# Performance work log

Measured on AMD Instinct MI355X. Metric: run time of the kernel, lower is better.

## Reference

```python
import jax, jax.numpy as jnp
import numpy as np

MAX_BOXES_PER_IMAGE = 200
NMS_IOU_THRESHOLD = 0.45
CONFIDENCE_THRESHOLD = 0.01
NEG = jnp.float32(-1e9)

B, N, C = 32, 24564, 81  # batch, anchors, classes (incl background)


def setup_inputs() -> dict:
    key = jax.random.key(0)
    k1, k2, k3 = jax.random.split(key, 3)
    logits = jax.random.normal(k1, (B, N, 4 + C), dtype=jnp.float32)
    # anchors in corner format [x0, y0, x1, y1], valid boxes in [0,1]
    centers = jax.random.uniform(k2, (N, 2), dtype=jnp.float32)
    sizes = jax.random.uniform(k3, (N, 2), dtype=jnp.float32) * 0.3 + 0.02
    anchors = jnp.clip(jnp.concatenate([centers - sizes / 2, centers + sizes / 2], axis=-1), 0.0, 1.0)
    return {"logits": logits, "anchors": anchors}


def decode_boxes(loc, anchors):
    # anchors [N,4] corners -> center/size; loc [B,N,4] offsets (no variance scaling, per source)
    cxcy = (anchors[:, 2:4] + anchors[:, 0:2]) / 2  # [N,2]
    wh = anchors[:, 2:4] - anchors[:, 0:2]          # [N,2]
    ctr = loc[..., 0:2] * wh + cxcy                 # [B,N,2]
    sz = jnp.exp(loc[..., 2:4]) * wh                # [B,N,2]
    boxes = jnp.concatenate([ctr - sz / 2, ctr + sz / 2], axis=-1)
    return jnp.clip(boxes, 0.0, 1.0)


def nms_single(boxes, scores):
    # boxes [N,4] corners, scores [N] (already -inf for background / below-threshold)
    area = (boxes[:, 2] - boxes[:, 0]) * (boxes[:, 3] - boxes[:, 1])

    def step(s, _):
        i = jnp.argmax(s)
        keep = s[i] > NEG / 2
        b = boxes[i]
        lt = jnp.maximum(b[:2], boxes[:, :2])
        rb = jnp.minimum(b[2:], boxes[:, 2:])
        whi = jnp.clip(rb - lt, 0.0)
        inter = whi[:, 0] * whi[:, 1]
        iou = inter / (area[i] + area - inter + 1e-9)
        s = jnp.where(iou > NMS_IOU_THRESHOLD, NEG, s).at[i].set(NEG)
        return s, (i, keep)

    _, (idx, keep) = jax.lax.scan(step, scores, None, length=MAX_BOXES_PER_IMAGE)
    return idx, keep  # [M], [M]


def reference(logits, anchors):
    loc = logits[..., :4]
    cls = jax.nn.softmax(logits[..., 4:], axis=-1)          # [B,N,C]
    scores = jnp.max(cls, axis=-1)                           # [B,N]
    classes = jnp.argmax(cls, axis=-1)                       # [B,N]
    boxes = decode_boxes(loc, anchors)                       # [B,N,4]
    # emulate boolean_mask(classes != 0) + score_threshold by masking scores
    valid = (classes != 0) & (scores >= CONFIDENCE_THRESHOLD)
    masked = jnp.where(valid, scores, NEG)
    idx, keep = jax.vmap(nms_single)(boxes, masked)          # [B,M]
    det_boxes = jax.vmap(lambda b, i: b[i])(boxes, idx) * keep[..., None].astype(boxes.dtype)
    det_scores = jax.vmap(lambda s, i: s[i])(scores, idx) * keep.astype(scores.dtype)
    det_classes = jax.vmap(lambda c, i: c[i])(classes, idx) * keep.astype(classes.dtype)
    det_num = jnp.sum(keep, axis=-1).astype(jnp.int32)
    return det_boxes, det_classes, det_scores, det_num
```

## Files before the change

### kernel.cpp

```cpp
#include <hip/hip_runtime.h>

#define Bn 32
#define Nn 24564
#define MAXB 200
#define NBIN 2048
#define CH 2048
#define INVK 0xFFFFFFFFu

typedef unsigned long long u64;
typedef unsigned int u32;

__device__ inline double fast_exp_d(double x) {
  const double LOG2E = 1.4426950408889634074;
  const double LN2   = 0.69314718055994530942;
  double t = x * LOG2E;
  double fi = floor(t + 0.5);
  double f = (t - fi) * LN2;
  double p = 2.505210838544172e-8;
  p = p * f + 2.755731922398589e-7;
  p = p * f + 2.7557319223985893e-6;
  p = p * f + 2.48015873015873e-5;
  p = p * f + 1.984126984126984e-4;
  p = p * f + 1.3888888888888889e-3;
  p = p * f + 8.333333333333333e-3;
  p = p * f + 4.1666666666666664e-2;
  p = p * f + 1.6666666666666666e-1;
  p = p * f + 0.5;
  p = p * f + 1.0;
  p = p * f + 1.0;
  long long e = (long long)fi;
  return p * __longlong_as_double((e + 1023LL) << 52);
}

__device__ inline double clip01(double v) {
  return v < 0.0 ? 0.0 : (v > 1.0 ? 1.0 : v);
}

__global__ __launch_bounds__(256) void r1_score(const float* __restrict__ logits,
                                                u32* __restrict__ keyA) {
  __shared__ float lds[64 * 85];
  const int tid = threadIdx.x;
  const int bx = blockIdx.x;
  const int b = bx / 384;
  const int n0 = (bx % 384) << 6;
  int cnt = Nn - n0;
  cnt = cnt > 64 ? 64 : cnt;
  const int nf4 = (cnt * 85) >> 2;
  const float4* src = reinterpret_cast<const float4*>(logits + ((size_t)b * Nn + n0) * 85);
  float4* dst = reinterpret_cast<float4*>(lds);
  for (int i = tid; i < nf4; i += 256) dst[i] = src[i];
  __syncthreads();

  const int g = tid >> 2;
  const int s = tid & 3;
  if (g < cnt) {
    const float* row = lds + g * 85;
    float mx = -1e30f; int ai = 1000;
    for (int c = s; c < 81; c += 4) {
      float v = row[4 + c];
      if (v > mx) { mx = v; ai = c; }
    }
    #pragma unroll
    for (int d = 1; d <= 2; d <<= 1) {
      float om = __shfl_xor(mx, d);
      int oi = __shfl_xor(ai, d);
      if (om > mx || (om == mx && oi < ai)) { mx = om; ai = oi; }
    }
    float sum = 0.f;
    for (int c = s; c < 81; c += 4) sum += __expf(row[4 + c] - mx);
    sum += __shfl_xor(sum, 1);
    sum += __shfl_xor(sum, 2);
    if (s == 0) {
      float sc = 1.0f / sum;
      u32 kv = INVK;
      if (ai != 0 && sc >= 0.00985f) kv = ~__float_as_uint(sc);
      keyA[(size_t)b * Nn + n0 + g] = kv;
    }
  }
}

__global__ __launch_bounds__(1024) void r2_selnms(const float* __restrict__ logits,
                                                  const float* __restrict__ anchors,
                                                  const u32* __restrict__ keyA,
                                                  double* __restrict__ boxesd,
                                                  int* __restrict__ clsd,
                                                  float* __restrict__ out) {
  __shared__ int hist[NBIN];
  __shared__ int wsum[16];
  __shared__ int clist[CH];
  __shared__ u64 ekeys[CH];
  __shared__ double bb[64][4];
  __shared__ u64 awv[16];
  __shared__ double selBox[MAXB][4];
  __shared__ double selArea[MAXB];
  __shared__ float selScore[MAXB];
  __shared__ int selIdx[MAXB];
  __shared__ int sBinHi, sCnt, sS;

  const int b = blockIdx.x;
  const int tid = threadIdx.x;
  const int lane = tid & 63, wid = tid >> 6;
  const u32* kb = keyA + (size_t)b * Nn;

  for (int i = tid; i < NBIN; i += 1024) hist[i] = 0;
  if (tid == 0) sS = 0;
  __syncthreads();
  for (int i = tid; i < Nn; i += 1024) {
    u32 kv = kb[i];
    u32 bin = (kv - 0xC0000000u) >> 15;
    if (bin < NBIN) atomicAdd(&hist[bin], 1);
  }
  __syncthreads();

  int h0 = hist[2 * tid], h1 = hist[2 * tid + 1];
  int v = h0 + h1;
  int iv = v;
  #pragma unroll
  for (int d = 1; d < 64; d <<= 1) {
    int t = __shfl_up(iv, d);
    if (lane >= d) iv += t;
  }
  if (lane == 63) wsum[wid] = iv;
  __syncthreads();
  if (tid < 16) {
    int w = wsum[tid];
    #pragma unroll
    for (int d = 1; d < 16; d <<= 1) {
      int t = __shfl_up(w, d);
      if ((int)tid >= d) w += t;
    }
    wsum[tid] = w;
  }
  __syncthreads();
  int excl = iv - v + (wid > 0 ? wsum[wid - 1] : 0);
  hist[2 * tid] = excl + h0;
  hist[2 * tid + 1] = excl + h0 + h1;
  __syncthreads();
  const int totalValid = hist[NBIN - 1];

  int binLo = -1, scanBase = 0;
  for (;;) {
    if (sS >= MAXB || scanBase >= totalValid) break;
    if (tid == 0) { sBinHi = binLo; sCnt = 0; }
    __syncthreads();
    {
      const int limit = scanBase + CH;
      int loc = -1;
      if (hist[2 * tid] <= limit) loc = 2 * tid;
      if (hist[2 * tid + 1] <= limit) loc = 2 * tid + 1;
      if (loc > binLo) atomicMax(&sBinHi, loc);
    }
    __syncthreads();
    int binHi = sBinHi;
    if (binHi == binLo) binHi = binLo + 1;

    for (int i0 = 0; i0 < Nn; i0 += 1024) {
      int i = i0 + tid;
      bool pred = false;
      if (i < Nn) {
        u32 kv = kb[i];
        int bin = (int)((kv - 0xC0000000u) >> 15);
        pred = (bin > binLo) && (bin <= binHi);
      }
      u64 m = __ballot(pred);
      int base = 0;
      if (lane == 0 && m) base = atomicAdd(&sCnt, (int)__popcll(m));
      base = __shfl(base, 0);
      if (pred) {
        int off = (int)__popcll(m & ((1ULL << lane) - 1ULL));
        int p = base + off;
        if (p < CH) clist[p] = i;
      }
    }
    __syncthreads();
    int count = sCnt; count = count > CH ? CH : count;
    for (int i = tid; i < CH; i += 1024) ekeys[i] = ~0ULL;
    __syncthreads();

    {
      const int g = tid >> 2, s = tid & 3;
      #pragma unroll 1
      for (int pass = 0; pass < CH / 256; ++pass) {
        int slot = pass * 256 + g;
        if (slot < count) {
          const int n = clist[slot];
          const float* row = logits + ((size_t)b * Nn + n) * 85;
          float rv[21];
          float mx = -1e30f; int ai = 1000;
          #pragma unroll
          for (int q = 0; q < 21; ++q) {
            int cc = s + 4 * q;
            float vv = (cc < 81) ? row[4 + cc] : -1e30f;
            rv[q] = vv;
            if (cc < 81 && vv > mx) { mx = vv; ai = cc; }
          }
          #pragma unroll
          for (int d = 1; d <= 2; d <<= 1) {
            float om = __shfl_xor(mx, d);
            int oi = __shfl_xor(ai, d);
            if (om > mx || (om == mx && oi < ai)) { mx = om; ai = oi; }
          }
          double sum = 0.0;
          #pragma unroll
          for (int q = 0; q < 21; ++q) {
            if (s + 4 * q < 81) sum += fast_exp_d((double)rv[q] - (double)mx);
          }
          sum += __shfl_xor(sum, 1);
          sum += __shfl_xor(sum, 2);
          if (s == 0) {
            u64 K = ~0ULL;
            double score = 1.0 / sum;
            if (ai != 0 && score >= 0.01) {
              float4 a4 = reinterpret_cast<const float4*>(anchors)[n];
              double ax1 = a4.x, ay1 = a4.y, ax2 = a4.z, ay2 = a4.w;
              double cx = (ax2 + ax1) * 0.5, cy = (ay2 + ay1) * 0.5;
              double ww = ax2 - ax1, hh = ay2 - ay1;
              double ctrx = (double)row[0] * ww + cx;
              double ctry = (double)row[1] * hh + cy;
              double szx = fast_exp_d((double)row[2]) * ww;
              double szy = fast_exp_d((double)row[3]) * hh;
              double* bp = boxesd + (size_t)(b * Nn + n) * 4;
              bp[0] = clip01(ctrx - szx * 0.5);
              bp[1] = clip01(ctry - szy * 0.5);
              bp[2] = clip01(ctrx + szx * 0.5);
              bp[3] = clip01(ctry + szy * 0.5);
              clsd[b * Nn + n] = ai;
              u64 sb = (u64)__double_as_longlong(score);
              u64 e4 = (sb >> 52) - 1015ULL;
              u64 mant45 = (sb & ((1ULL << 52) - 1)) >> 7;
              u64 flip = (~((e4 << 45) | mant45)) & ((1ULL << 49) - 1);
              K = (flip << 15) | (u64)n;
            }
            ekeys[slot] = K;
          }
        }
      }
    }
    __syncthreads();

    for (int k = 2; k <= CH; k <<= 1) {
      for (int j = k >> 1; j >= 1; j >>= 1) {
        int l = ((tid & ~(j - 1)) << 1) | (tid & (j - 1));
        int r = l | j;
        bool up = ((l & k) == 0);
        u64 a = ekeys[l], bbv = ekeys[r];
        if ((a > bbv) == up) { ekeys[l] = bbv; ekeys[r] = a; }
        __syncthreads();
      }
    }

    const double THR = 0.45;
    int pos = 0;
    for (;;) {
      int S = sS;
      if (S >= MAXB || pos >= CH) break;
      u64 K = ekeys[pos + lane];
      bool valid = (K != ~0ULL);
      if (!__any(valid)) break;

      if (tid < 256) {
        int c = tid >> 2, comp = tid & 3;
        u64 Kc = ekeys[pos + c];
        double vv = 0.0;
        if (Kc != ~0ULL)
          vv = boxesd[(size_t)(b * Nn + (int)(Kc & 0x7FFF)) * 4 + comp];
        bb[c][comp] = vv;
      }
      __syncthreads();

      double cx1 = bb[lane][0], cy1 = bb[lane][1];
      double cx2 = bb[lane][2], cy2 = bb[lane][3];
      double carea = (cx2 - cx1) * (cy2 - cy1);
      bool aliveL = true;
      for (int k = wid; k < S; k += 16) {
        double ltx = fmax(selBox[k][0], cx1), lty = fmax(selBox[k][1], cy1);
        double rbx = fmin(selBox[k][2], cx2), rby = fmin(selBox[k][3], cy2);
        double w = rbx - ltx; w = w < 0 ? 0 : w;
        double h = rby - lty; h = h < 0 ? 0 : h;
        double inter = w * h;
        double denom = selArea[k] + carea - inter + 1e-9;
        if (inter > THR * denom) aliveL = false;
      }
      u64 aw = __ballot(aliveL);
      if (lane == 0) awv[wid] = aw;
      __syncthreads();

      if (tid < 64) {
        u64 alive = __ballot(valid);
        #pragma unroll
        for (int w = 0; w < 16; ++w) alive &= awv[w];
        u64 m = alive;
        int Sl = S;
        while (m != 0 && Sl < MAXB) {
          int j = __ffsll((unsigned long long)m) - 1;
          double jx1 = bb[j][0], jy1 = bb[j][1], jx2 = bb[j][2], jy2 = bb[j][3];
          double jar = (jx2 - jx1) * (jy2 - jy1);
          u64 Kj = ekeys[pos + j];
          if (lane == 0) {
            u64 key49 = (~(Kj >> 15)) & ((1ULL << 49) - 1);
            u64 e = (key49 >> 45) + 1015ULL;
            u64 mant = (key49 & ((1ULL << 45) - 1)) << 7;
            selBox[Sl][0] = jx1; selBox[Sl][1] = jy1;
            selBox[Sl][2] = jx2; selBox[Sl][3] = jy2;
            selArea[Sl] = jar;
            selScore[Sl] = (float)__longlong_as_double((long long)((e << 52) | mant));
            selIdx[Sl] = (int)(Kj & 0x7FFF);
          }
          Sl++;
          m &= ~(1ULL << j);
          double ltx = fmax(jx1, cx1), lty = fmax(jy1, cy1);
          double rbx = fmin(jx2, cx2), rby = fmin(jy2, cy2);
          double w = rbx - ltx; w = w < 0 ? 0 : w;
          double h = rby - lty; h = h < 0 ? 0 : h;
          double inter = w * h;
          double denom = jar + carea - inter + 1e-9;
          m &= ~__ballot(inter > THR * denom);
        }
        if (lane == 0) sS = Sl;
      }
      __syncthreads();
      pos += 64;
    }
    __syncthreads();
    scanBase = hist[binHi];
    binLo = binHi;
  }

  const int S = sS;
  float* det_boxes = out;
  float* det_classes = out + Bn * MAXB * 4;
  float* det_scores = out + Bn * MAXB * 4 + Bn * MAXB;
  float* det_num = out + Bn * MAXB * 4 + 2 * Bn * MAXB;
  for (int k = tid; k < MAXB; k += 1024) {
    int o = b * MAXB + k;
    if (k < S) {
      det_boxes[o * 4 + 0] = (float)selBox[k][0];
      det_boxes[o * 4 + 1] = (float)selBox[k][1];
      det_boxes[o * 4 + 2] = (float)selBox[k][2];
      det_boxes[o * 4 + 3] = (float)selBox[k][3];
      det_classes[o] = (float)clsd[b * Nn + selIdx[k]];
      det_scores[o] = selScore[k];
    } else {
      det_boxes[o * 4 + 0] = 0.f; det_boxes[o * 4 + 1] = 0.f;
      det_boxes[o * 4 + 2] = 0.f; det_boxes[o * 4 + 3] = 0.f;
      det_classes[o] = 0.f;
      det_scores[o] = 0.f;
    }
  }
  if (tid == 0) det_num[b] = (float)S;
}

extern "C" void kernel_launch(void* const* d_in, const int* in_sizes, int n_in,
                              void* d_out, int out_size, void* d_ws, size_t ws_size,
                              hipStream_t stream) {
  const float* logits = (const float*)d_in[0];
  const float* anchors = (const float*)d_in[1];
  float* out = (float*)d_out;
  char* ws = (char*)d_ws;

  double* boxesd = (double*)ws;
  size_t off = (size_t)Bn * Nn * 4 * sizeof(double);
  int* clsd = (int*)(ws + off);  off += (size_t)Bn * Nn * sizeof(int);
  u32* keyA = (u32*)(ws + off);

  r1_score <<<dim3(Bn * 384), dim3(256),  0, stream>>>(logits, keyA);
  r2_selnms<<<dim3(Bn),       dim3(1024), 0, stream>>>(logits, anchors, keyA,
                                                       boxesd, clsd, out);
}
```

Measured before the change: 187.9 us.

## Split per-image select/NMS kernel into multi-stage grid-parallel pipeline

```diff
diff --git a/kernel.cpp b/kernel.cpp
--- a/kernel.cpp
+++ b/kernel.cpp
@@ -5,6 +5,8 @@
 #define MAXB 200
 #define NBIN 2048
 #define CH 2048
+#define NCHK 4
+#define CHTOT (NCHK * CH)
 #define INVK 0xFFFFFFFFu
 
 typedef unsigned long long u64;
@@ -36,7 +38,7 @@
   return v < 0.0 ? 0.0 : (v > 1.0 ? 1.0 : v);
 }
 
-__global__ __launch_bounds__(256) void r1_score(const float* __restrict__ logits,
+__global__ __launch_bounds__(256) void s1_score(const float* __restrict__ logits,
                                                 u32* __restrict__ keyA) {
   __shared__ float lds[64 * 85];
   const int tid = threadIdx.x;
@@ -79,39 +81,43 @@
   }
 }
 
-__global__ __launch_bounds__(1024) void r2_selnms(const float* __restrict__ logits,
-                                                  const float* __restrict__ anchors,
-                                                  const u32* __restrict__ keyA,
-                                                  double* __restrict__ boxesd,
-                                                  int* __restrict__ clsd,
-                                                  float* __restrict__ out) {
+__global__ __launch_bounds__(256) void s2_hist(const u32* __restrict__ keyA,
+                                               int* __restrict__ histG) {
+  __shared__ int hl[NBIN];
+  const int tid = threadIdx.x;
+  const int bx = blockIdx.x;
+  const int b = bx >> 3;
+  const int sl = (bx & 7) * 3072;
+  for (int i = tid; i < NBIN; i += 256) hl[i] = 0;
+  __syncthreads();
+  const u32* kb = keyA + (size_t)b * Nn;
+  for (int k = 0; k < 12; ++k) {
+    int i = sl + k * 256 + tid;
+    if (i < Nn) {
+      u32 kv = kb[i];
+      u32 bin = (kv - 0xC0000000u) >> 15;
+      if (bin < NBIN) atomicAdd(&hl[bin], 1);
+    }
+  }
+  __syncthreads();
+  for (int i = tid; i < NBIN; i += 256) {
+    int v = hl[i];
+    if (v) atomicAdd(&histG[b * NBIN + i], v);
+  }
+}
+
+__global__ __launch_bounds__(1024) void s3_cut(const int* __restrict__ histG,
+                                               int* __restrict__ chunkIdG,
+                                               int* __restrict__ chunkCntG) {
   __shared__ int hist[NBIN];
   __shared__ int wsum[16];
-  __shared__ int clist[CH];
-  __shared__ u64 ekeys[CH];
-  __shared__ double bb[64][4];
-  __shared__ u64 awv[16];
-  __shared__ double selBox[MAXB][4];
-  __shared__ double selArea[MAXB];
-  __shared__ float selScore[MAXB];
-  __shared__ int selIdx[MAXB];
-  __shared__ int sBinHi, sCnt, sS;
-
+  __shared__ int sBinHi;
   const int b = blockIdx.x;
   const int tid = threadIdx.x;
   const int lane = tid & 63, wid = tid >> 6;
-  const u32* kb = keyA + (size_t)b * Nn;
-
-  for (int i = tid; i < NBIN; i += 1024) hist[i] = 0;
-  if (tid == 0) sS = 0;
-  __syncthreads();
-  for (int i = tid; i < Nn; i += 1024) {
-    u32 kv = kb[i];
-    u32 bin = (kv - 0xC0000000u) >> 15;
-    if (bin < NBIN) atomicAdd(&hist[bin], 1);
-  }
-  __syncthreads();
-
+  hist[2 * tid] = histG[b * NBIN + 2 * tid];
+  hist[2 * tid + 1] = histG[b * NBIN + 2 * tid + 1];
+  __syncthreads();
   int h0 = hist[2 * tid], h1 = hist[2 * tid + 1];
   int v = h0 + h1;
   int iv = v;
@@ -136,140 +142,203 @@
   hist[2 * tid] = excl + h0;
   hist[2 * tid + 1] = excl + h0 + h1;
   __syncthreads();
-  const int totalValid = hist[NBIN - 1];
-
-  int binLo = -1, scanBase = 0;
-  for (;;) {
-    if (sS >= MAXB || scanBase >= totalValid) break;
-    if (tid == 0) { sBinHi = binLo; sCnt = 0; }
-    __syncthreads();
-    {
-      const int limit = scanBase + CH;
-      int loc = -1;
-      if (hist[2 * tid] <= limit) loc = 2 * tid;
-      if (hist[2 * tid + 1] <= limit) loc = 2 * tid + 1;
-      if (loc > binLo) atomicMax(&sBinHi, loc);
-    }
+
+  int cid0 = 255, cid1 = 255;
+  int binLo = -1, base = 0;
+  for (int c = 0; c < NCHK; ++c) {
+    if (tid == 0) sBinHi = binLo;
+    __syncthreads();
+    const int limit = base + CH;
+    int loc = -1;
+    if (hist[2 * tid] <= limit) loc = 2 * tid;
+    if (hist[2 * tid + 1] <= limit) loc = 2 * tid + 1;
+    if (loc > binLo) atomicMax(&sBinHi, loc);
     __syncthreads();
     int binHi = sBinHi;
     if (binHi == binLo) binHi = binLo + 1;
-
-    for (int i0 = 0; i0 < Nn; i0 += 1024) {
-      int i = i0 + tid;
-      bool pred = false;
-      if (i < Nn) {
-        u32 kv = kb[i];
-        int bin = (int)((kv - 0xC0000000u) >> 15);
-        pred = (bin > binLo) && (bin <= binHi);
-      }
-      u64 m = __ballot(pred);
+    if (2 * tid > binLo && 2 * tid <= binHi) cid0 = c;
+    if (2 * tid + 1 > binLo && 2 * tid + 1 <= binHi) cid1 = c;
+    base = hist[(binHi < NBIN ? binHi : NBIN - 1)];
+    binLo = binHi;
+    __syncthreads();
+  }
+  chunkIdG[b * NBIN + 2 * tid] = cid0;
+  chunkIdG[b * NBIN + 2 * tid + 1] = cid1;
+  if (tid < NCHK) chunkCntG[b * NCHK + tid] = 0;
+}
+
+__global__ __launch_bounds__(256) void s4_compact(const u32* __restrict__ keyA,
+                                                  const int* __restrict__ chunkIdG,
+                                                  int* __restrict__ chunkCntG,
+                                                  int* __restrict__ clist) {
+  const int tid = threadIdx.x;
+  const int bx = blockIdx.x;
+  const int b = bx / 96;
+  const int i = ((bx % 96) << 8) + tid;
+  const int lane = tid & 63;
+  int c = 255;
+  if (i < Nn) {
+    u32 kv = keyA[(size_t)b * Nn + i];
+    u32 bin = (kv - 0xC0000000u) >> 15;
+    if (bin < NBIN) c = chunkIdG[b * NBIN + bin];
+  }
+  #pragma unroll
+  for (int cc = 0; cc < NCHK; ++cc) {
+    bool pred = (c == cc);
+    u64 m = __ballot(pred);
+    if (m) {
       int base = 0;
-      if (lane == 0 && m) base = atomicAdd(&sCnt, (int)__popcll(m));
+      if (lane == 0) base = atomicAdd(&chunkCntG[b * NCHK + cc], (int)__popcll(m));
       base = __shfl(base, 0);
       if (pred) {
         int off = (int)__popcll(m & ((1ULL << lane) - 1ULL));
         int p = base + off;
-        if (p < CH) clist[p] = i;
-      }
-    }
-    __syncthreads();
-    int count = sCnt; count = count > CH ? CH : count;
-    for (int i = tid; i < CH; i += 1024) ekeys[i] = ~0ULL;
-    __syncthreads();
-
-    {
-      const int g = tid >> 2, s = tid & 3;
-      #pragma unroll 1
-      for (int pass = 0; pass < CH / 256; ++pass) {
-        int slot = pass * 256 + g;
-        if (slot < count) {
-          const int n = clist[slot];
-          const float* row = logits + ((size_t)b * Nn + n) * 85;
-          float rv[21];
-          float mx = -1e30f; int ai = 1000;
-          #pragma unroll
-          for (int q = 0; q < 21; ++q) {
-            int cc = s + 4 * q;
-            float vv = (cc < 81) ? row[4 + cc] : -1e30f;
-            rv[q] = vv;
-            if (cc < 81 && vv > mx) { mx = vv; ai = cc; }
-          }
-          #pragma unroll
-          for (int d = 1; d <= 2; d <<= 1) {
-            float om = __shfl_xor(mx, d);
-            int oi = __shfl_xor(ai, d);
-            if (om > mx || (om == mx && oi < ai)) { mx = om; ai = oi; }
-          }
-          double sum = 0.0;
-          #pragma unroll
-          for (int q = 0; q < 21; ++q) {
-            if (s + 4 * q < 81) sum += fast_exp_d((double)rv[q] - (double)mx);
-          }
-          sum += __shfl_xor(sum, 1);
-          sum += __shfl_xor(sum, 2);
-          if (s == 0) {
-            u64 K = ~0ULL;
-            double score = 1.0 / sum;
-            if (ai != 0 && score >= 0.01) {
-              float4 a4 = reinterpret_cast<const float4*>(anchors)[n];
-              double ax1 = a4.x, ay1 = a4.y, ax2 = a4.z, ay2 = a4.w;
-              double cx = (ax2 + ax1) * 0.5, cy = (ay2 + ay1) * 0.5;
-              double ww = ax2 - ax1, hh = ay2 - ay1;
-              double ctrx = (double)row[0] * ww + cx;
-              double ctry = (double)row[1] * hh + cy;
-              double szx = fast_exp_d((double)row[2]) * ww;
-              double szy = fast_exp_d((double)row[3]) * hh;
-              double* bp = boxesd + (size_t)(b * Nn + n) * 4;
-              bp[0] = clip01(ctrx - szx * 0.5);
-              bp[1] = clip01(ctry - szy * 0.5);
-              bp[2] = clip01(ctrx + szx * 0.5);
-              bp[3] = clip01(ctry + szy * 0.5);
-              clsd[b * Nn + n] = ai;
-              u64 sb = (u64)__double_as_longlong(score);
-              u64 e4 = (sb >> 52) - 1015ULL;
-              u64 mant45 = (sb & ((1ULL << 52) - 1)) >> 7;
-              u64 flip = (~((e4 << 45) | mant45)) & ((1ULL << 49) - 1);
-              K = (flip << 15) | (u64)n;
-            }
-            ekeys[slot] = K;
-          }
+        if (p < CH) clist[b * CHTOT + cc * CH + p] = i;
+      }
+    }
+  }
+}
+
+__global__ __launch_bounds__(256) void s5_rescore(const float* __restrict__ logits,
+                                                  const float* __restrict__ anchors,
+                                                  const int* __restrict__ clist,
+                                                  const int* __restrict__ chunkCntG,
+                                                  double* __restrict__ boxesd,
+                                                  int* __restrict__ clsd,
+                                                  u64* __restrict__ ekeysG) {
+  const int tid = threadIdx.x;
+  const int bx = blockIdx.x;
+  const int b = bx >> 7;
+  const int blk = bx & 127;
+  const int c = blk >> 5;
+  const int sb = (blk & 31) << 6;
+  int cnt = chunkCntG[b * NCHK + c];
+  cnt = cnt > CH ? CH : cnt;
+  const int g = tid >> 2, s = tid & 3;
+  const int slot = sb + g;
+  u64 K = ~0ULL;
+  if (slot < cnt) {
+    const int n = clist[b * CHTOT + c * CH + slot];
+    const float* row = logits + ((size_t)b * Nn + n) * 85;
+    float rv[21];
+    float mx = -1e30f; int ai = 1000;
+    #pragma unroll
+    for (int q = 0; q < 21; ++q) {
+      int cc = s + 4 * q;
+      float vv = (cc < 81) ? row[4 + cc] : -1e30f;
+      rv[q] = vv;
+      if (cc < 81 && vv > mx) { mx = vv; ai = cc; }
+    }
+    #pragma unroll
+    for (int d = 1; d <= 2; d <<= 1) {
+      float om = __shfl_xor(mx, d);
+      int oi = __shfl_xor(ai, d);
+      if (om > mx || (om == mx && oi < ai)) { mx = om; ai = oi; }
+    }
+    double sum = 0.0;
+    #pragma unroll
+    for (int q = 0; q < 21; ++q) {
+      if (s + 4 * q < 81) sum += fast_exp_d((double)rv[q] - (double)mx);
+    }
+    sum += __shfl_xor(sum, 1);
+    sum += __shfl_xor(sum, 2);
+    if (s == 0) {
+      double score = 1.0 / sum;
+      if (ai != 0 && score >= 0.01) {
+        float4 a4 = reinterpret_cast<const float4*>(anchors)[n];
+        double ax1 = a4.x, ay1 = a4.y, ax2 = a4.z, ay2 = a4.w;
+        double cx = (ax2 + ax1) * 0.5, cy = (ay2 + ay1) * 0.5;
+        double ww = ax2 - ax1, hh = ay2 - ay1;
+        double ctrx = (double)row[0] * ww + cx;
+        double ctry = (double)row[1] * hh + cy;
+        double szx = fast_exp_d((double)row[2]) * ww;
+        double szy = fast_exp_d((double)row[3]) * hh;
+        double* bp = boxesd + (size_t)(b * Nn + n) * 4;
+        bp[0] = clip01(ctrx - szx * 0.5);
+        bp[1] = clip01(ctry - szy * 0.5);
+        bp[2] = clip01(ctrx + szx * 0.5);
+        bp[3] = clip01(ctry + szy * 0.5);
+        clsd[b * Nn + n] = ai;
+        u64 sb2 = (u64)__double_as_longlong(score);
+        u64 e4 = (sb2 >> 52) - 1015ULL;
+        u64 mant45 = (sb2 & ((1ULL << 52) - 1)) >> 7;
+        u64 flip = (~((e4 << 45) | mant45)) & ((1ULL << 49) - 1);
+        K = (flip << 15) | (u64)n;
+      }
+    }
+  }
+  if (s == 0) ekeysG[b * CHTOT + c * CH + slot] = K;
+}
+
+__global__ __launch_bounds__(1024) void s6_sortnms(const u64* __restrict__ ekeysG,
+                                                   const int* __restrict__ chunkCntG,
+                                                   const double* __restrict__ boxesd,
+                                                   const int* __restrict__ clsd,
+                                                   float* __restrict__ out) {
+  __shared__ u64 ek[CH];
+  __shared__ double bbuf[2][64][4];
+  __shared__ u64 awv[16];
+  __shared__ double selBox[MAXB][4];
+  __shared__ double selArea[MAXB];
+  __shared__ float selScore[MAXB];
+  __shared__ int selIdx[MAXB];
+  __shared__ int sS;
+  const int b = blockIdx.x;
+  const int tid = threadIdx.x;
+  const int lane = tid & 63, wid = tid >> 6;
+  const double THR = 0.45;
+  if (tid == 0) sS = 0;
+  __syncthreads();
+
+  for (int c = 0; c < NCHK; ++c) {
+    if (sS >= MAXB) break;
+    int cnt = chunkCntG[b * NCHK + c];
+    cnt = cnt > CH ? CH : cnt;
+    if (cnt == 0) break;
+    for (int i = tid; i < CH; i += 1024) ek[i] = ekeysG[b * CHTOT + c * CH + i];
+    __syncthreads();
+
+    int P2 = 64;
+    while (P2 < cnt) P2 <<= 1;
+    for (int k = 2; k <= P2; k <<= 1) {
+      for (int j = k >> 1; j >= 1; j >>= 1) {
+        if (tid < (P2 >> 1)) {
+          int l = ((tid & ~(j - 1)) << 1) | (tid & (j - 1));
+          int r = l | j;
+          bool up = ((l & k) == 0);
+          u64 a = ek[l], bbv = ek[r];
+          if ((a > bbv) == up) { ek[l] = bbv; ek[r] = a; }
         }
-      }
-    }
-    __syncthreads();
-
-    for (int k = 2; k <= CH; k <<= 1) {
-      for (int j = k >> 1; j >= 1; j >>= 1) {
-        int l = ((tid & ~(j - 1)) << 1) | (tid & (j - 1));
-        int r = l | j;
-        bool up = ((l & k) == 0);
-        u64 a = ekeys[l], bbv = ekeys[r];
-        if ((a > bbv) == up) { ekeys[l] = bbv; ekeys[r] = a; }
         __syncthreads();
       }
     }
 
-    const double THR = 0.45;
-    int pos = 0;
+    int pos = 0, bf = 0;
+    if (tid < 256) {
+      int ci = tid >> 2, comp = tid & 3;
+      u64 Kc = ek[ci];
+      double vv = 0.0;
+      if (Kc != ~0ULL) vv = boxesd[(size_t)(b * Nn + (int)(Kc & 0x7FFF)) * 4 + comp];
+      bbuf[0][ci][comp] = vv;
+    }
+    __syncthreads();
     for (;;) {
       int S = sS;
       if (S >= MAXB || pos >= CH) break;
-      u64 K = ekeys[pos + lane];
+      u64 K = ek[pos + lane];
       bool valid = (K != ~0ULL);
       if (!__any(valid)) break;
 
-      if (tid < 256) {
-        int c = tid >> 2, comp = tid & 3;
-        u64 Kc = ekeys[pos + c];
+      if (tid < 256 && pos + 64 < CH) {
+        int ci = tid >> 2, comp = tid & 3;
+        u64 Kc = ek[pos + 64 + ci];
         double vv = 0.0;
-        if (Kc != ~0ULL)
-          vv = boxesd[(size_t)(b * Nn + (int)(Kc & 0x7FFF)) * 4 + comp];
-        bb[c][comp] = vv;
-      }
-      __syncthreads();
-
-      double cx1 = bb[lane][0], cy1 = bb[lane][1];
-      double cx2 = bb[lane][2], cy2 = bb[lane][3];
+        if (Kc != ~0ULL) vv = boxesd[(size_t)(b * Nn + (int)(Kc & 0x7FFF)) * 4 + comp];
+        bbuf[bf ^ 1][ci][comp] = vv;
+      }
+
+      double cx1 = bbuf[bf][lane][0], cy1 = bbuf[bf][lane][1];
+      double cx2 = bbuf[bf][lane][2], cy2 = bbuf[bf][lane][3];
       double carea = (cx2 - cx1) * (cy2 - cy1);
       bool aliveL = true;
       for (int k = wid; k < S; k += 16) {
@@ -293,9 +362,10 @@
         int Sl = S;
         while (m != 0 && Sl < MAXB) {
           int j = __ffsll((unsigned long long)m) - 1;
-          double jx1 = bb[j][0], jy1 = bb[j][1], jx2 = bb[j][2], jy2 = bb[j][3];
+          double jx1 = bbuf[bf][j][0], jy1 = bbuf[bf][j][1];
+          double jx2 = bbuf[bf][j][2], jy2 = bbuf[bf][j][3];
           double jar = (jx2 - jx1) * (jy2 - jy1);
-          u64 Kj = ekeys[pos + j];
+          u64 Kj = ek[pos + j];
           if (lane == 0) {
             u64 key49 = (~(Kj >> 15)) & ((1ULL << 49) - 1);
             u64 e = (key49 >> 45) + 1015ULL;
@@ -319,11 +389,10 @@
         if (lane == 0) sS = Sl;
       }
       __syncthreads();
+      bf ^= 1;
       pos += 64;
     }
     __syncthreads();
-    scanBase = hist[binHi];
-    binLo = binHi;
   }
 
   const int S = sS;
@@ -360,10 +429,20 @@
 
   double* boxesd = (double*)ws;
   size_t off = (size_t)Bn * Nn * 4 * sizeof(double);
-  int* clsd = (int*)(ws + off);  off += (size_t)Bn * Nn * sizeof(int);
-  u32* keyA = (u32*)(ws + off);
-
-  r1_score <<<dim3(Bn * 384), dim3(256),  0, stream>>>(logits, keyA);
-  r2_selnms<<<dim3(Bn),       dim3(1024), 0, stream>>>(logits, anchors, keyA,
-                                                       boxesd, clsd, out);
-}
+  int* clsd    = (int*)(ws + off);  off += (size_t)Bn * Nn * sizeof(int);
+  u32* keyA    = (u32*)(ws + off);  off += (size_t)Bn * Nn * sizeof(u32);
+  int* histG   = (int*)(ws + off);  off += (size_t)Bn * NBIN * sizeof(int);
+  int* chunkId = (int*)(ws + off);  off += (size_t)Bn * NBIN * sizeof(int);
+  int* chunkCnt= (int*)(ws + off);  off += (size_t)Bn * NCHK * sizeof(int);
+  int* clist   = (int*)(ws + off);  off += (size_t)Bn * CHTOT * sizeof(int);
+  u64* ekeysG  = (u64*)(ws + off);
+
+  hipMemsetAsync(histG, 0, (size_t)Bn * NBIN * sizeof(int), stream);
+  s1_score  <<<dim3(Bn * 384), dim3(256),  0, stream>>>(logits, keyA);
+  s2_hist   <<<dim3(Bn * 8),   dim3(256),  0, stream>>>(keyA, histG);
+  s3_cut    <<<dim3(Bn),       dim3(1024), 0, stream>>>(histG, chunkId, chunkCnt);
+  s4_compact<<<dim3(Bn * 96),  dim3(256),  0, stream>>>(keyA, chunkId, chunkCnt, clist);
+  s5_rescore<<<dim3(Bn * 128), dim3(256),  0, stream>>>(logits, anchors, clist, chunkCnt,
+                                                        boxesd, clsd, ekeysG);
+  s6_sortnms<<<dim3(Bn),       dim3(1024), 0, stream>>>(ekeysG, chunkCnt, boxesd, clsd, out);
+}
```

Result: slower. 367.7 us (+95.7%).

## Split histogram into parallel kernel, keep candidate boxes in LDS, parallelize NMS kill masks

Applied to the files above, without the earlier changes.

```diff
diff --git a/kernel.cpp b/kernel.cpp
--- a/kernel.cpp
+++ b/kernel.cpp
@@ -5,6 +5,7 @@
 #define MAXB 200
 #define NBIN 2048
 #define CH 2048
+#define NCHK 4
 #define INVK 0xFFFFFFFFu
 
 typedef unsigned long long u64;
@@ -36,7 +37,7 @@
   return v < 0.0 ? 0.0 : (v > 1.0 ? 1.0 : v);
 }
 
-__global__ __launch_bounds__(256) void r1_score(const float* __restrict__ logits,
+__global__ __launch_bounds__(256) void v1_score(const float* __restrict__ logits,
                                                 u32* __restrict__ keyA) {
   __shared__ float lds[64 * 85];
   const int tid = threadIdx.x;
@@ -79,40 +80,68 @@
   }
 }
 
-__global__ __launch_bounds__(1024) void r2_selnms(const float* __restrict__ logits,
+__global__ __launch_bounds__(256) void v2_hist(const u32* __restrict__ keyA,
+                                               int* __restrict__ histP) {
+  __shared__ int hl[NBIN];
+  const int tid = threadIdx.x;
+  const int bx = blockIdx.x;
+  const int b = bx >> 3;
+  const int p = bx & 7;
+  const int sl = p * 3072;
+  for (int i = tid; i < NBIN; i += 256) hl[i] = 0;
+  __syncthreads();
+  const u32* kb = keyA + (size_t)b * Nn;
+  for (int k = 0; k < 12; ++k) {
+    int i = sl + k * 256 + tid;
+    if (i < Nn) {
+      u32 kv = kb[i];
+      u32 bin = (kv - 0xC0000000u) >> 15;
+      if (bin < NBIN) atomicAdd(&hl[bin], 1);
+    }
+  }
+  __syncthreads();
+  int* dst = histP + ((size_t)(b << 3) + p) * NBIN;
+  for (int i = tid; i < NBIN; i += 256) dst[i] = hl[i];
+}
+
+__global__ __launch_bounds__(1024) void v3_selnms(const int* __restrict__ histP,
+                                                  const u32* __restrict__ keyA,
+                                                  const float* __restrict__ logits,
                                                   const float* __restrict__ anchors,
-                                                  const u32* __restrict__ keyA,
-                                                  double* __restrict__ boxesd,
-                                                  int* __restrict__ clsd,
                                                   float* __restrict__ out) {
   __shared__ int hist[NBIN];
+  __shared__ int chunkIdL[NBIN];
   __shared__ int wsum[16];
+  __shared__ int sBinHi, sCnt, sS;
+  __shared__ u64 ek[CH];
+  __shared__ u32 slotP[CH];
   __shared__ int clist[CH];
-  __shared__ u64 ekeys[CH];
-  __shared__ double bb[64][4];
+  __shared__ double cbox[CH][4];
+  __shared__ unsigned char clsL[CH];
   __shared__ u64 awv[16];
+  __shared__ u64 killm[64];
   __shared__ double selBox[MAXB][4];
   __shared__ double selArea[MAXB];
   __shared__ float selScore[MAXB];
-  __shared__ int selIdx[MAXB];
-  __shared__ int sBinHi, sCnt, sS;
+  __shared__ float selCls[MAXB];
 
   const int b = blockIdx.x;
   const int tid = threadIdx.x;
   const int lane = tid & 63, wid = tid >> 6;
   const u32* kb = keyA + (size_t)b * Nn;
-
-  for (int i = tid; i < NBIN; i += 1024) hist[i] = 0;
+  const double THR = 0.45;
+
+  int h0 = 0, h1 = 0;
+  #pragma unroll
+  for (int p = 0; p < 8; ++p) {
+    const int* src = histP + ((size_t)(b << 3) + p) * NBIN;
+    h0 += src[2 * tid];
+    h1 += src[2 * tid + 1];
+  }
+  chunkIdL[2 * tid] = 255;
+  chunkIdL[2 * tid + 1] = 255;
   if (tid == 0) sS = 0;
-  __syncthreads();
-  for (int i = tid; i < Nn; i += 1024) {
-    u32 kv = kb[i];
-    u32 bin = (kv - 0xC0000000u) >> 15;
-    if (bin < NBIN) atomicAdd(&hist[bin], 1);
-  }
-  __syncthreads();
-
-  int h0 = hist[2 * tid], h1 = hist[2 * tid + 1];
+
   int v = h0 + h1;
   int iv = v;
   #pragma unroll
@@ -136,60 +165,71 @@
   hist[2 * tid] = excl + h0;
   hist[2 * tid + 1] = excl + h0 + h1;
   __syncthreads();
-  const int totalValid = hist[NBIN - 1];
-
-  int binLo = -1, scanBase = 0;
-  for (;;) {
-    if (sS >= MAXB || scanBase >= totalValid) break;
-    if (tid == 0) { sBinHi = binLo; sCnt = 0; }
-    __syncthreads();
-    {
-      const int limit = scanBase + CH;
+
+  {
+    int binLo = -1, cumBase = 0;
+    for (int c = 0; c < NCHK; ++c) {
+      if (tid == 0) sBinHi = binLo;
+      __syncthreads();
+      const int limit = cumBase + CH;
       int loc = -1;
       if (hist[2 * tid] <= limit) loc = 2 * tid;
       if (hist[2 * tid + 1] <= limit) loc = 2 * tid + 1;
       if (loc > binLo) atomicMax(&sBinHi, loc);
-    }
+      __syncthreads();
+      int binHi = sBinHi;
+      if (binHi == binLo) binHi = binLo + 1;
+      if (2 * tid > binLo && 2 * tid <= binHi) chunkIdL[2 * tid] = c;
+      if (2 * tid + 1 > binLo && 2 * tid + 1 <= binHi) chunkIdL[2 * tid + 1] = c;
+      cumBase = hist[(binHi < NBIN ? binHi : NBIN - 1)];
+      binLo = binHi;
+      __syncthreads();
+    }
+  }
+
+  for (int c = 0; c < NCHK; ++c) {
+    if (sS >= MAXB) break;
+    if (tid == 0) sCnt = 0;
+    for (int i = tid; i < CH; i += 1024) { ek[i] = ~0ULL; slotP[i] = (u32)i; }
     __syncthreads();
-    int binHi = sBinHi;
-    if (binHi == binLo) binHi = binLo + 1;
 
     for (int i0 = 0; i0 < Nn; i0 += 1024) {
       int i = i0 + tid;
       bool pred = false;
       if (i < Nn) {
         u32 kv = kb[i];
-        int bin = (int)((kv - 0xC0000000u) >> 15);
-        pred = (bin > binLo) && (bin <= binHi);
+        u32 bin = (kv - 0xC0000000u) >> 15;
+        pred = (bin < NBIN) && (chunkIdL[bin] == c);
       }
       u64 m = __ballot(pred);
-      int base = 0;
-      if (lane == 0 && m) base = atomicAdd(&sCnt, (int)__popcll(m));
-      base = __shfl(base, 0);
-      if (pred) {
-        int off = (int)__popcll(m & ((1ULL << lane) - 1ULL));
-        int p = base + off;
-        if (p < CH) clist[p] = i;
+      if (m) {
+        int base = 0;
+        if (lane == 0) base = atomicAdd(&sCnt, (int)__popcll(m));
+        base = __shfl(base, 0);
+        if (pred) {
+          int off = (int)__popcll(m & ((1ULL << lane) - 1ULL));
+          int p = base + off;
+          if (p < CH) clist[p] = i;
+        }
       }
     }
     __syncthreads();
-    int count = sCnt; count = count > CH ? CH : count;
-    for (int i = tid; i < CH; i += 1024) ekeys[i] = ~0ULL;
-    __syncthreads();
+    int cnt = sCnt; cnt = cnt > CH ? CH : cnt;
+    if (cnt == 0) break;
 
     {
-      const int g = tid >> 2, s = tid & 3;
+      const int g = tid >> 2, s4 = tid & 3;
       #pragma unroll 1
       for (int pass = 0; pass < CH / 256; ++pass) {
         int slot = pass * 256 + g;
-        if (slot < count) {
+        if (slot < cnt) {
           const int n = clist[slot];
           const float* row = logits + ((size_t)b * Nn + n) * 85;
           float rv[21];
           float mx = -1e30f; int ai = 1000;
           #pragma unroll
           for (int q = 0; q < 21; ++q) {
-            int cc = s + 4 * q;
+            int cc = s4 + 4 * q;
             float vv = (cc < 81) ? row[4 + cc] : -1e30f;
             rv[q] = vv;
             if (cc < 81 && vv > mx) { mx = vv; ai = cc; }
@@ -203,11 +243,11 @@
           double sum = 0.0;
           #pragma unroll
           for (int q = 0; q < 21; ++q) {
-            if (s + 4 * q < 81) sum += fast_exp_d((double)rv[q] - (double)mx);
+            if (s4 + 4 * q < 81) sum += fast_exp_d((double)rv[q] - (double)mx);
           }
           sum += __shfl_xor(sum, 1);
           sum += __shfl_xor(sum, 2);
-          if (s == 0) {
+          if (s4 == 0) {
             u64 K = ~0ULL;
             double score = 1.0 / sum;
             if (ai != 0 && score >= 0.01) {
@@ -219,58 +259,56 @@
               double ctry = (double)row[1] * hh + cy;
               double szx = fast_exp_d((double)row[2]) * ww;
               double szy = fast_exp_d((double)row[3]) * hh;
-              double* bp = boxesd + (size_t)(b * Nn + n) * 4;
-              bp[0] = clip01(ctrx - szx * 0.5);
-              bp[1] = clip01(ctry - szy * 0.5);
-              bp[2] = clip01(ctrx + szx * 0.5);
-              bp[3] = clip01(ctry + szy * 0.5);
-              clsd[b * Nn + n] = ai;
-              u64 sb = (u64)__double_as_longlong(score);
-              u64 e4 = (sb >> 52) - 1015ULL;
-              u64 mant45 = (sb & ((1ULL << 52) - 1)) >> 7;
+              cbox[slot][0] = clip01(ctrx - szx * 0.5);
+              cbox[slot][1] = clip01(ctry - szy * 0.5);
+              cbox[slot][2] = clip01(ctrx + szx * 0.5);
+              cbox[slot][3] = clip01(ctry + szy * 0.5);
+              clsL[slot] = (unsigned char)ai;
+              u64 sb2 = (u64)__double_as_longlong(score);
+              u64 e4 = (sb2 >> 52) - 1015ULL;
+              u64 mant45 = (sb2 & ((1ULL << 52) - 1)) >> 7;
               u64 flip = (~((e4 << 45) | mant45)) & ((1ULL << 49) - 1);
               K = (flip << 15) | (u64)n;
             }
-            ekeys[slot] = K;
+            ek[slot] = K;
           }
         }
       }
     }
     __syncthreads();
 
-    for (int k = 2; k <= CH; k <<= 1) {
+    int P2 = 64;
+    while (P2 < cnt) P2 <<= 1;
+    for (int k = 2; k <= P2; k <<= 1) {
       for (int j = k >> 1; j >= 1; j >>= 1) {
-        int l = ((tid & ~(j - 1)) << 1) | (tid & (j - 1));
-        int r = l | j;
-        bool up = ((l & k) == 0);
-        u64 a = ekeys[l], bbv = ekeys[r];
-        if ((a > bbv) == up) { ekeys[l] = bbv; ekeys[r] = a; }
+        if (tid < (P2 >> 1)) {
+          int l = ((tid & ~(j - 1)) << 1) | (tid & (j - 1));
+          int r = l | j;
+          bool up = ((l & k) == 0);
+          u64 a = ek[l], bv = ek[r];
+          if ((a > bv) == up) {
+            ek[l] = bv; ek[r] = a;
+            u32 t = slotP[l]; slotP[l] = slotP[r]; slotP[r] = t;
+          }
+        }
         __syncthreads();
       }
     }
 
-    const double THR = 0.45;
     int pos = 0;
     for (;;) {
       int S = sS;
       if (S >= MAXB || pos >= CH) break;
-      u64 K = ekeys[pos + lane];
+      u64 K = ek[pos + lane];
       bool valid = (K != ~0ULL);
       if (!__any(valid)) break;
-
-      if (tid < 256) {
-        int c = tid >> 2, comp = tid & 3;
-        u64 Kc = ekeys[pos + c];
-        double vv = 0.0;
-        if (Kc != ~0ULL)
-          vv = boxesd[(size_t)(b * Nn + (int)(Kc & 0x7FFF)) * 4 + comp];
-        bb[c][comp] = vv;
-      }
-      __syncthreads();
-
-      double cx1 = bb[lane][0], cy1 = bb[lane][1];
-      double cx2 = bb[lane][2], cy2 = bb[lane][3];
+      int slt = (int)slotP[pos + lane];
+      double cx1 = valid ? cbox[slt][0] : 0.0;
+      double cy1 = valid ? cbox[slt][1] : 0.0;
+      double cx2 = valid ? cbox[slt][2] : 0.0;
+      double cy2 = valid ? cbox[slt][3] : 0.0;
       double carea = (cx2 - cx1) * (cy2 - cy1);
+
       bool aliveL = true;
       for (int k = wid; k < S; k += 16) {
         double ltx = fmax(selBox[k][0], cx1), lty = fmax(selBox[k][1], cy1);
@@ -283,6 +321,27 @@
       }
       u64 aw = __ballot(aliveL);
       if (lane == 0) awv[wid] = aw;
+
+      #pragma unroll
+      for (int q = 0; q < 4; ++q) {
+        int j = (wid << 2) | q;
+        u64 Kj = ek[pos + j];
+        int sj = (int)slotP[pos + j];
+        bool jv = (Kj != ~0ULL);
+        double jx1 = jv ? cbox[sj][0] : 0.0;
+        double jy1 = jv ? cbox[sj][1] : 0.0;
+        double jx2 = jv ? cbox[sj][2] : 0.0;
+        double jy2 = jv ? cbox[sj][3] : 0.0;
+        double jar = (jx2 - jx1) * (jy2 - jy1);
+        double ltx = fmax(jx1, cx1), lty = fmax(jy1, cy1);
+        double rbx = fmin(jx2, cx2), rby = fmin(jy2, cy2);
+        double w = rbx - ltx; w = w < 0 ? 0 : w;
+        double h = rby - lty; h = h < 0 ? 0 : h;
+        double inter = w * h;
+        double denom = jar + carea - inter + 1e-9;
+        u64 km = __ballot(inter > THR * denom);
+        if (lane == 0) killm[j] = km;
+      }
       __syncthreads();
 
       if (tid < 64) {
@@ -293,28 +352,23 @@
         int Sl = S;
         while (m != 0 && Sl < MAXB) {
           int j = __ffsll((unsigned long long)m) - 1;
-          double jx1 = bb[j][0], jy1 = bb[j][1], jx2 = bb[j][2], jy2 = bb[j][3];
-          double jar = (jx2 - jx1) * (jy2 - jy1);
-          u64 Kj = ekeys[pos + j];
           if (lane == 0) {
+            u64 Kj = ek[pos + j];
+            int sj = (int)slotP[pos + j];
+            double jx1 = cbox[sj][0], jy1 = cbox[sj][1];
+            double jx2 = cbox[sj][2], jy2 = cbox[sj][3];
             u64 key49 = (~(Kj >> 15)) & ((1ULL << 49) - 1);
             u64 e = (key49 >> 45) + 1015ULL;
             u64 mant = (key49 & ((1ULL << 45) - 1)) << 7;
             selBox[Sl][0] = jx1; selBox[Sl][1] = jy1;
             selBox[Sl][2] = jx2; selBox[Sl][3] = jy2;
-            selArea[Sl] = jar;
+            selArea[Sl] = (jx2 - jx1) * (jy2 - jy1);
             selScore[Sl] = (float)__longlong_as_double((long long)((e << 52) | mant));
-            selIdx[Sl] = (int)(Kj & 0x7FFF);
+            selCls[Sl] = (float)clsL[sj];
           }
           Sl++;
           m &= ~(1ULL << j);
-          double ltx = fmax(jx1, cx1), lty = fmax(jy1, cy1);
-          double rbx = fmin(jx2, cx2), rby = fmin(jy2, cy2);
-          double w = rbx - ltx; w = w < 0 ? 0 : w;
-          double h = rby - lty; h = h < 0 ? 0 : h;
-          double inter = w * h;
-          double denom = jar + carea - inter + 1e-9;
-          m &= ~__ballot(inter > THR * denom);
+          m &= ~killm[j];
         }
         if (lane == 0) sS = Sl;
       }
@@ -322,8 +376,6 @@
       pos += 64;
     }
     __syncthreads();
-    scanBase = hist[binHi];
-    binLo = binHi;
   }
 
   const int S = sS;
@@ -338,7 +390,7 @@
       det_boxes[o * 4 + 1] = (float)selBox[k][1];
       det_boxes[o * 4 + 2] = (float)selBox[k][2];
       det_boxes[o * 4 + 3] = (float)selBox[k][3];
-      det_classes[o] = (float)clsd[b * Nn + selIdx[k]];
+      det_classes[o] = selCls[k];
       det_scores[o] = selScore[k];
     } else {
       det_boxes[o * 4 + 0] = 0.f; det_boxes[o * 4 + 1] = 0.f;
@@ -358,12 +410,10 @@
   float* out = (float*)d_out;
   char* ws = (char*)d_ws;
 
-  double* boxesd = (double*)ws;
-  size_t off = (size_t)Bn * Nn * 4 * sizeof(double);
-  int* clsd = (int*)(ws + off);  off += (size_t)Bn * Nn * sizeof(int);
-  u32* keyA = (u32*)(ws + off);
-
-  r1_score <<<dim3(Bn * 384), dim3(256),  0, stream>>>(logits, keyA);
-  r2_selnms<<<dim3(Bn),       dim3(1024), 0, stream>>>(logits, anchors, keyA,
-                                                       boxesd, clsd, out);
-}
+  u32* keyA  = (u32*)ws;
+  int* histP = (int*)(ws + (size_t)Bn * Nn * sizeof(u32));
+
+  v1_score <<<dim3(Bn * 384), dim3(256),  0, stream>>>(logits, keyA);
+  v2_hist  <<<dim3(Bn * 8),   dim3(256),  0, stream>>>(keyA, histP);
+  v3_selnms<<<dim3(Bn),       dim3(1024), 0, stream>>>(histP, keyA, logits, anchors, out);
+}
```

Measured after the change: 206.9 us. 10.1% more time.
